# Optimization experiments

Hardware: AMD Instinct MI355X
Metric: run time of the kernel (lower is better)

## Reference

```python
import jax, jax.numpy as jnp
import numpy as np

SAMPLES = 8    # batch of sets
N = 1024       # set size == rows of the permutation-closed index matrix
K = 16         # number of distinct weight-sharing groups
M = N // K     # columns per group per row (rectangular splits)
CI = 128       # channels_in
CO = 256       # channels_out


def setup_inputs() -> dict:
    key = jax.random.key(0)
    kx, kw = jax.random.split(key)
    x = jax.random.normal(kx, (SAMPLES, N, CI), dtype=jnp.float32)
    # weightParameter: [k, channels_out, channels_in]
    W = jax.random.normal(kw, (K, CO, CI), dtype=jnp.float32)
    # Rebuild the circulant group structure that __init__ derives from
    # running_weight_matrix: row j of `indices` is roll(base, j), so the
    # columns of group g in row j are (pos_g + j) mod N.
    base = np.repeat(np.arange(K), M)                      # indices row 0, [N]
    pos = np.stack([np.where(base == g)[0] for g in range(K)])  # [K, M]
    splits = (pos[:, None, :] + np.arange(N)[None, :, None]) % N  # [K, N, M]
    return {"x": x, "W": W, "splits": jnp.asarray(splits, jnp.int32)}


def reference(x, W, splits):
    # sum-pool branch: result = sum_g ( sum_m x[:, splits[g]] ) @ W[g].T
    def body(acc, group):
        w, sp = group                      # w: [CO, CI], sp: [N, M]
        pooled = x[:, sp].sum(axis=2)      # gather [S, N, M, CI] -> [S, N, CI]
        return acc + jnp.einsum('snc,oc->sno', pooled, w), None

    init = jnp.zeros((x.shape[0], splits.shape[1], W.shape[1]), dtype=x.dtype)
    out, _ = jax.lax.scan(body, init, (W, splits))
    return out                             # [S, N, CO]
```

## Files before the change

### kernel.cpp

```cpp
#include <hip/hip_runtime.h>
#include <hip/hip_bf16.h>

#define S_   8
#define N_   1024
#define KG_  16
#define MW_  64
#define CI_  128
#define CO_  256

typedef __attribute__((ext_vector_type(8))) short bf16x8;
typedef __attribute__((ext_vector_type(4))) float f32x4;

__global__ __launch_bounds__(256) void wconv_kernel(const float* __restrict__ W,
                                                    __hip_bfloat16* __restrict__ Wb) {
    const int i = (blockIdx.x * 256 + threadIdx.x) * 4;
    const float4 v = *(const float4*)&W[i];
    Wb[i + 0] = __float2bfloat16(v.x);
    Wb[i + 1] = __float2bfloat16(v.y);
    Wb[i + 2] = __float2bfloat16(v.z);
    Wb[i + 3] = __float2bfloat16(v.w);
}

__global__ __launch_bounds__(256) void win_kernel(const float* __restrict__ x,
                                                  __hip_bfloat16* __restrict__ win) {
    __shared__ float lds[96][CI_];
    const int b   = blockIdx.x;
    const int s   = b >> 5;
    const int t0  = (b & 31) << 5;
    const float* xs = x + (size_t)s * N_ * CI_;
    const int tid = threadIdx.x;

    for (int e = tid * 4; e < 96 * CI_; e += 256 * 4) {
        const int r = e >> 7;
        const int c = e & (CI_ - 1);
        *(float4*)&lds[r][c] = *(const float4*)&xs[((t0 + r) & (N_ - 1)) * CI_ + c];
    }
    __syncthreads();

    const int c  = tid & (CI_ - 1);
    const int tb = (tid >> 7) << 4;
    float s0 = 0.f, s1 = 0.f, s2 = 0.f, s3 = 0.f;
    #pragma unroll
    for (int m = 0; m < MW_; m += 4) {
        s0 += lds[tb + m + 0][c];
        s1 += lds[tb + m + 1][c];
        s2 += lds[tb + m + 2][c];
        s3 += lds[tb + m + 3][c];
    }
    float w = (s0 + s1) + (s2 + s3);
    __hip_bfloat16* wo = win + (size_t)s * N_ * CI_;
    wo[(t0 + tb) * CI_ + c] = __float2bfloat16(w);
    #pragma unroll
    for (int t = 1; t < 16; ++t) {
        w += lds[tb + t - 1 + MW_][c] - lds[tb + t - 1][c];
        wo[(t0 + tb + t) * CI_ + c] = __float2bfloat16(w);
    }
}

#define BKE  128
#define ASZ  (128 * BKE)
#define BSZ  (64  * BKE)

__global__ __launch_bounds__(256) void gemm_kernel(const __hip_bfloat16* __restrict__ winb,
                                                   const __hip_bfloat16* __restrict__ Wb,
                                                   float* __restrict__ out) {
    __shared__ __align__(16) unsigned short Alds[2 * ASZ];
    __shared__ __align__(16) unsigned short Blds[2 * BSZ];

    const int tid = threadIdx.x;
    const int l   = tid & 63;
    const int wv  = tid >> 6;
    const int mb  = blockIdx.x;
    const int s   = mb >> 3;
    const int n0  = (mb & 7) << 7;
    const int o0  = blockIdx.y << 6;

    const int wm = wv >> 1;
    const int wn = wv & 1;
    const int fr = l & 15;
    const int kq = l >> 4;

    const unsigned short* winp = (const unsigned short*)winb + (size_t)s * N_ * CI_;
    const unsigned short* Wp   = (const unsigned short*)Wb;

    const int rl = l >> 4;
    const int ps = l & 15;

    f32x4 acc[4][2];
    #pragma unroll
    for (int i = 0; i < 4; ++i)
        #pragma unroll
        for (int j = 0; j < 2; ++j)
            acc[i][j] = f32x4{0.f, 0.f, 0.f, 0.f};

    auto stage = [&](int g, int buf) {
        unsigned short* Ab = &Alds[buf * ASZ];
        unsigned short* Bb = &Blds[buf * BSZ];
        #pragma unroll
        for (int q = 0; q < 8; ++q) {
            const int rb   = wv * 32 + q * 4;
            const int row  = rb + rl;
            const int ss   = ps ^ (row & 7);
            const int grow = (n0 + (g << 6) + row) & (N_ - 1);
            const unsigned short* src = winp + grow * CI_ + ss * 8;
            __builtin_amdgcn_global_load_lds((const __attribute__((address_space(1))) void*)src,
                                             (__attribute__((address_space(3))) void*)(Ab + rb * BKE),
                                             16, 0, 0);
        }
        #pragma unroll
        for (int q = 0; q < 4; ++q) {
            const int rb  = wv * 16 + q * 4;
            const int row = rb + rl;
            const int ss  = ps ^ (row & 7);
            const unsigned short* src = Wp + ((g * CO_ + o0 + row) * CI_) + ss * 8;
            __builtin_amdgcn_global_load_lds((const __attribute__((address_space(1))) void*)src,
                                             (__attribute__((address_space(3))) void*)(Bb + rb * BKE),
                                             16, 0, 0);
        }
    };

    stage(0, 0);
    __syncthreads();

    for (int g = 0; g < KG_; ++g) {
        const int cur = g & 1;
        if (g + 1 < KG_) stage(g + 1, cur ^ 1);

        const unsigned short* Ab = &Alds[cur * ASZ];
        const unsigned short* Bb = &Blds[cur * BSZ];
        #pragma unroll
        for (int ksub = 0; ksub < 4; ++ksub) {
            const int sl = ksub * 4 + kq;
            bf16x8 af[4], bfr[2];
            #pragma unroll
            for (int i = 0; i < 4; ++i) {
                const int row = wm * 64 + i * 16 + fr;
                af[i] = *(const bf16x8*)&Ab[row * BKE + ((sl ^ (row & 7)) * 8)];
            }
            #pragma unroll
            for (int j = 0; j < 2; ++j) {
                const int col = wn * 32 + j * 16 + fr;
                bfr[j] = *(const bf16x8*)&Bb[col * BKE + ((sl ^ (col & 7)) * 8)];
            }
            #pragma unroll
            for (int i = 0; i < 4; ++i)
                #pragma unroll
                for (int j = 0; j < 2; ++j)
                    acc[i][j] = __builtin_amdgcn_mfma_f32_16x16x32_bf16(af[i], bfr[j], acc[i][j], 0, 0, 0);
        }
        __syncthreads();
    }

    float* op = out + ((size_t)(s * N_ + n0 + wm * 64) * CO_) + o0 + wn * 32;
    #pragma unroll
    for (int i = 0; i < 4; ++i)
        #pragma unroll
        for (int j = 0; j < 2; ++j)
            #pragma unroll
            for (int r = 0; r < 4; ++r)
                op[(i * 16 + kq * 4 + r) * CO_ + j * 16 + fr] = acc[i][j][r];
}

extern "C" void kernel_launch(void* const* d_in, const int* in_sizes, int n_in,
                              void* d_out, int out_size, void* d_ws, size_t ws_size,
                              hipStream_t stream) {
    const float* x = (const float*)d_in[0];
    const float* W = (const float*)d_in[1];

    __hip_bfloat16* winb = (__hip_bfloat16*)d_ws;
    __hip_bfloat16* Wbb  = (__hip_bfloat16*)((char*)d_ws +
                              (size_t)S_ * N_ * CI_ * sizeof(__hip_bfloat16));
    float* out = (float*)d_out;

    wconv_kernel<<<512, 256, 0, stream>>>(W, Wbb);
    win_kernel<<<256, 256, 0, stream>>>(x, winb);
    gemm_kernel<<<dim3(64, 4), 256, 0, stream>>>(winb, Wbb, out);
}
```

Measured before the change: 95.29 us.

## Fuse weight conversion into window kernel and halve GEMM K-tile with vmcnt pipelining

The separate weight-to-bf16 conversion kernel is folded into the window-sum kernel, which saves one launch. The GEMM now stages 64-wide K chunks (32 steps instead of 16), halving LDS use. It also replaces __syncthreads with explicit vmcnt waits and s_barrier, so the next tile's async loads stay in flight during compute. The risks are more barriers per step and a hand-tuned vmcnt count that must match the number of issued loads.

```diff
diff --git a/kernel.cpp b/kernel.cpp
--- a/kernel.cpp
+++ b/kernel.cpp
@@ -11,24 +11,34 @@
 typedef __attribute__((ext_vector_type(8))) short bf16x8;
 typedef __attribute__((ext_vector_type(4))) float f32x4;
 
-__global__ __launch_bounds__(256) void wconv_kernel(const float* __restrict__ W,
-                                                    __hip_bfloat16* __restrict__ Wb) {
-    const int i = (blockIdx.x * 256 + threadIdx.x) * 4;
-    const float4 v = *(const float4*)&W[i];
-    Wb[i + 0] = __float2bfloat16(v.x);
-    Wb[i + 1] = __float2bfloat16(v.y);
-    Wb[i + 2] = __float2bfloat16(v.z);
-    Wb[i + 3] = __float2bfloat16(v.w);
-}
-
 __global__ __launch_bounds__(256) void win_kernel(const float* __restrict__ x,
-                                                  __hip_bfloat16* __restrict__ win) {
+                                                  const float* __restrict__ W,
+                                                  __hip_bfloat16* __restrict__ win,
+                                                  __hip_bfloat16* __restrict__ Wb) {
     __shared__ float lds[96][CI_];
     const int b   = blockIdx.x;
+    const int tid = threadIdx.x;
+
+    {
+        const int wi = (b * 256 + tid) * 8;
+        const float4 v0 = *(const float4*)&W[wi];
+        const float4 v1 = *(const float4*)&W[wi + 4];
+        union { unsigned short u[8]; uint4 v; } o;
+        __hip_bfloat16 h;
+        h = __float2bfloat16(v0.x); o.u[0] = *(unsigned short*)&h;
+        h = __float2bfloat16(v0.y); o.u[1] = *(unsigned short*)&h;
+        h = __float2bfloat16(v0.z); o.u[2] = *(unsigned short*)&h;
+        h = __float2bfloat16(v0.w); o.u[3] = *(unsigned short*)&h;
+        h = __float2bfloat16(v1.x); o.u[4] = *(unsigned short*)&h;
+        h = __float2bfloat16(v1.y); o.u[5] = *(unsigned short*)&h;
+        h = __float2bfloat16(v1.z); o.u[6] = *(unsigned short*)&h;
+        h = __float2bfloat16(v1.w); o.u[7] = *(unsigned short*)&h;
+        *(uint4*)&Wb[wi] = o.v;
+    }
+
     const int s   = b >> 5;
     const int t0  = (b & 31) << 5;
     const float* xs = x + (size_t)s * N_ * CI_;
-    const int tid = threadIdx.x;
 
     for (int e = tid * 4; e < 96 * CI_; e += 256 * 4) {
         const int r = e >> 7;
@@ -57,34 +67,33 @@
     }
 }
 
-#define BKE  128
-#define ASZ  (128 * BKE)
-#define BSZ  (64  * BKE)
+#define BKE  64
+#define AST  (128 * BKE)
+#define BST  (64  * BKE)
+#define KSTEPS 32
 
 __global__ __launch_bounds__(256) void gemm_kernel(const __hip_bfloat16* __restrict__ winb,
                                                    const __hip_bfloat16* __restrict__ Wb,
                                                    float* __restrict__ out) {
-    __shared__ __align__(16) unsigned short Alds[2 * ASZ];
-    __shared__ __align__(16) unsigned short Blds[2 * BSZ];
+    __shared__ __align__(16) unsigned short Alds[2 * AST];
+    __shared__ __align__(16) unsigned short Blds[2 * BST];
 
     const int tid = threadIdx.x;
     const int l   = tid & 63;
     const int wv  = tid >> 6;
-    const int mb  = blockIdx.x;
-    const int s   = mb >> 3;
-    const int n0  = (mb & 7) << 7;
+    const int s   = blockIdx.x >> 3;
+    const int n0  = (blockIdx.x & 7) << 7;
     const int o0  = blockIdx.y << 6;
 
     const int wm = wv >> 1;
     const int wn = wv & 1;
     const int fr = l & 15;
     const int kq = l >> 4;
+    const int rl = l >> 3;
+    const int ps = l & 7;
 
     const unsigned short* winp = (const unsigned short*)winb + (size_t)s * N_ * CI_;
     const unsigned short* Wp   = (const unsigned short*)Wb;
-
-    const int rl = l >> 4;
-    const int ps = l & 15;
 
     f32x4 acc[4][2];
     #pragma unroll
@@ -93,26 +102,29 @@
         for (int j = 0; j < 2; ++j)
             acc[i][j] = f32x4{0.f, 0.f, 0.f, 0.f};
 
-    auto stage = [&](int g, int buf) {
-        unsigned short* Ab = &Alds[buf * ASZ];
-        unsigned short* Bb = &Blds[buf * BSZ];
+    auto stage = [&](int t, int buf) {
+        const int g  = t >> 1;
+        const int ch = (t & 1) << 6;
+        unsigned short* Ab = &Alds[buf * AST];
+        unsigned short* Bb = &Blds[buf * BST];
         #pragma unroll
-        for (int q = 0; q < 8; ++q) {
-            const int rb   = wv * 32 + q * 4;
-            const int row  = rb + rl;
-            const int ss   = ps ^ (row & 7);
-            const int grow = (n0 + (g << 6) + row) & (N_ - 1);
-            const unsigned short* src = winp + grow * CI_ + ss * 8;
+        for (int q = 0; q < 4; ++q) {
+            const int rb  = (wv * 4 + q) * 8;
+            const int row = rb + rl;
+            const int ss  = ps ^ (row & 7);
+            const unsigned short* src =
+                winp + (((n0 + (g << 6) + row) & (N_ - 1)) * CI_) + ch + ss * 8;
             __builtin_amdgcn_global_load_lds((const __attribute__((address_space(1))) void*)src,
                                              (__attribute__((address_space(3))) void*)(Ab + rb * BKE),
                                              16, 0, 0);
         }
         #pragma unroll
-        for (int q = 0; q < 4; ++q) {
-            const int rb  = wv * 16 + q * 4;
+        for (int q = 0; q < 2; ++q) {
+            const int rb  = (wv * 2 + q) * 8;
             const int row = rb + rl;
             const int ss  = ps ^ (row & 7);
-            const unsigned short* src = Wp + ((g * CO_ + o0 + row) * CI_) + ss * 8;
+            const unsigned short* src =
+                Wp + ((g * CO_ + o0 + row) * CI_) + ch + ss * 8;
             __builtin_amdgcn_global_load_lds((const __attribute__((address_space(1))) void*)src,
                                              (__attribute__((address_space(3))) void*)(Bb + rb * BKE),
                                              16, 0, 0);
@@ -120,18 +132,24 @@
     };
 
     stage(0, 0);
-    __syncthreads();
 
-    for (int g = 0; g < KG_; ++g) {
-        const int cur = g & 1;
-        if (g + 1 < KG_) stage(g + 1, cur ^ 1);
+    for (int t = 0; t < KSTEPS; ++t) {
+        const int cur = t & 1;
+        if (t < KSTEPS - 1) {
+            stage(t + 1, cur ^ 1);
+            asm volatile("s_waitcnt vmcnt(6)" ::: "memory");
+        } else {
+            asm volatile("s_waitcnt vmcnt(0)" ::: "memory");
+        }
+        __builtin_amdgcn_sched_barrier(0);
+        __builtin_amdgcn_s_barrier();
 
-        const unsigned short* Ab = &Alds[cur * ASZ];
-        const unsigned short* Bb = &Blds[cur * BSZ];
+        const unsigned short* Ab = &Alds[cur * AST];
+        const unsigned short* Bb = &Blds[cur * BST];
         #pragma unroll
-        for (int ksub = 0; ksub < 4; ++ksub) {
-            const int sl = ksub * 4 + kq;
-            bf16x8 af[4], bfr[2];
+        for (int ks = 0; ks < 2; ++ks) {
+            const int sl = ks * 4 + kq;
+            bf16x8 af[4], bfg[2];
             #pragma unroll
             for (int i = 0; i < 4; ++i) {
                 const int row = wm * 64 + i * 16 + fr;
@@ -140,15 +158,16 @@
             #pragma unroll
             for (int j = 0; j < 2; ++j) {
                 const int col = wn * 32 + j * 16 + fr;
-                bfr[j] = *(const bf16x8*)&Bb[col * BKE + ((sl ^ (col & 7)) * 8)];
+                bfg[j] = *(const bf16x8*)&Bb[col * BKE + ((sl ^ (col & 7)) * 8)];
             }
             #pragma unroll
             for (int i = 0; i < 4; ++i)
                 #pragma unroll
                 for (int j = 0; j < 2; ++j)
-                    acc[i][j] = __builtin_amdgcn_mfma_f32_16x16x32_bf16(af[i], bfr[j], acc[i][j], 0, 0, 0);
+                    acc[i][j] = __builtin_amdgcn_mfma_f32_16x16x32_bf16(af[i], bfg[j], acc[i][j], 0, 0, 0);
         }
-        __syncthreads();
+        __builtin_amdgcn_sched_barrier(0);
+        __builtin_amdgcn_s_barrier();
     }
 
     float* op = out + ((size_t)(s * N_ + n0 + wm * 64) * CO_) + o0 + wn * 32;
@@ -172,7 +191,6 @@
                               (size_t)S_ * N_ * CI_ * sizeof(__hip_bfloat16));
     float* out = (float*)d_out;
 
-    wconv_kernel<<<512, 256, 0, stream>>>(W, Wbb);
-    win_kernel<<<256, 256, 0, stream>>>(x, winb);
+    win_kernel<<<256, 256, 0, stream>>>(x, W, winb, Wbb);
     gemm_kernel<<<dim3(64, 4), 256, 0, stream>>>(winb, Wbb, out);
 }
```

Measured after the change: 98.21 us. 3.1% more time.
